# Kernel tuning notes

Hardware: AMD Instinct MI355X
Metric: run time of the kernel (lower is better)

The kernel has to match this reference:

```python
import jax, jax.numpy as jnp
import numpy as np

W_CUB = 0.1
W_CD = 1.0
W_EXT = 0.01
W_SPS = 0.01
THRED = 24.0
COS_EPS = 1e-4

# cube face buffers (6 faces x 3 coords)
MASK_PROJECT = jnp.array([[0,1,1],[0,1,1],[1,0,1],[1,0,1],[1,1,0],[1,1,0]], jnp.float32)
MASK_PLANE   = jnp.array([[1,0,0],[1,0,0],[0,1,0],[0,1,0],[0,0,1],[0,0,1]], jnp.float32)
CUBE_NORMAL  = jnp.array([[-1,0,0],[1,0,0],[0,-1,0],[0,1,0],[0,0,-1],[0,0,1]], jnp.float32)
# torch repeat(...,3,...) of [[-1,-1,-1],[1,1,1]] tiles it -> [c0,c1,c0,c1,c0,c1]
CUBE_PLANES6 = jnp.tile(jnp.array([[-1.,-1.,-1.],[1.,1.,1.]], jnp.float32), (3,1))


def setup_inputs():
    B, P, N, S = 4, 24, 3072, 128
    key = jax.random.key(0)
    ks = jax.random.split(key, 8)
    pc_inver = jax.random.normal(ks[0], (B, P, N, 3), jnp.float32)
    normals_inver = jax.random.normal(ks[1], (B, P, N, 3), jnp.float32)
    scale = jax.random.uniform(ks[2], (B, P, 3), jnp.float32) * 0.9 + 0.1
    shape = jax.random.uniform(ks[3], (B, P, 2), jnp.float32) * 1.3 + 0.2
    exist = jax.random.uniform(ks[4], (B, P, 1), jnp.float32) * 0.98 + 0.01
    assign_matrix = jax.nn.softmax(jax.random.normal(ks[5], (B, N, P), jnp.float32), axis=-1)
    etas = jax.random.uniform(ks[6], (B, P, S), jnp.float32, minval=-jnp.pi/2, maxval=jnp.pi/2)
    omegas = jax.random.uniform(ks[7], (B, P, S), jnp.float32, minval=-jnp.pi, maxval=jnp.pi)
    return dict(pc_inver=pc_inver, normals_inver=normals_inver, scale=scale,
                shape=shape, exist=exist, assign_matrix=assign_matrix,
                etas=etas, omegas=omegas)


def _fexp(x, p):
    return jnp.sign(x) * jnp.abs(x) ** p


def _sample_sq_points(scale, eps, etas, omegas):
    # scale (B,P,3), eps (B,P,2), etas/omegas (B,P,S) -> (B,P,S,3)
    etas = jnp.where(etas == 0, 1e-6, etas)
    omegas = jnp.where(omegas == 0, 1e-6, omegas)
    a1, a2, a3 = scale[..., 0:1], scale[..., 1:2], scale[..., 2:3]
    e1, e2 = eps[..., 0:1], eps[..., 1:2]
    ce, se = jnp.cos(etas), jnp.sin(etas)
    co, so = jnp.cos(omegas), jnp.sin(omegas)
    x = a1 * _fexp(ce, e1) * _fexp(co, e2)
    y = a2 * _fexp(ce, e1) * _fexp(so, e2)
    z = a3 * _fexp(se, e1)
    fix = lambda v: (jnp.where(v > 0, 1.0, -1.0)) * jnp.maximum(jnp.abs(v), 1e-6)
    return jnp.stack([fix(x), fix(y), fix(z)], -1)


def _cd_loss(pc_inver, scale, shape, exist, assign_matrix, etas, omegas):
    X = _sample_sq_points(scale, shape, etas, omegas)          # (B,P,S,3)
    diff = X[:, :, :, None, :] - pc_inver[:, :, None, :, :]    # (B,P,S,N,3)
    D = jnp.sum(diff * diff, -1)                               # (B,P,S,N)
    pcl2prim = jnp.min(D, axis=2)                              # (B,P,N)
    pcl_loss = jnp.mean(jnp.sum(jnp.swapaxes(pcl2prim, 1, 2) * assign_matrix, -1))
    prim2pcl = jnp.mean(jnp.min(D, axis=3), axis=-1)           # (B,P)
    e = exist[..., 0]
    prim_loss = jnp.mean(jnp.sum(prim2pcl * e, -1) / (jnp.sum(e, -1) + 1e-6))
    return pcl_loss, prim_loss


def _cuboid_loss(pc_inver, normals_inver, scale, assign_matrix):
    pc = jnp.swapaxes(pc_inver, 1, 2)        # (B,N,P,3)
    nrm = jnp.swapaxes(normals_inver, 1, 2)  # (B,N,P,3)
    n_norm = jnp.maximum(jnp.linalg.norm(nrm, axis=-1, keepdims=True), COS_EPS)
    cos = jnp.einsum('bnpc,fc->bnpf', nrm, CUBE_NORMAL) / n_norm  # ||cube_normal||=1
    idx = jnp.argmax(cos, axis=-1)           # (B,N,P)
    s = scale[:, None, :, None, :]           # (B,1,P,1,3)
    proj = pc[:, :, :, None, :] * MASK_PROJECT + (CUBE_PLANES6 * s) * MASK_PLANE  # (B,N,P,6,3)
    proj = jnp.clip(proj, -s, s)
    proj_sel = jnp.take_along_axis(proj, idx[..., None, None], axis=3)[..., 0, :]  # (B,N,P,3)
    d = jnp.sum((proj_sel - pc) ** 2, -1)    # (B,N,P)
    return jnp.mean(jnp.sum(d * assign_matrix, -1))


def _common_losses(assign_matrix, exist):
    gt = jax.lax.stop_gradient((jnp.sum(assign_matrix, 1) > THRED).astype(jnp.float32))  # (B,P)
    p = exist[..., 0]
    bce = -jnp.mean(gt * jnp.log(p) + (1.0 - gt) * jnp.log1p(-p))
    N = assign_matrix.shape[1]
    sps = jnp.mean(jnp.mean(jnp.sqrt(jnp.sum(assign_matrix, 1) / N + 0.01), -1) ** 2)
    return bce, sps


def reference(pc_inver, normals_inver, scale, shape, exist, assign_matrix, etas, omegas):
    cub = _cuboid_loss(pc_inver, normals_inver, scale, assign_matrix)
    pcl_loss, prim_loss = _cd_loss(pc_inver, scale, shape, exist, assign_matrix, etas, omegas)
    bce, sps = _common_losses(assign_matrix, exist)
    return W_CUB * cub + W_CD * (pcl_loss + prim_loss) + W_EXT * bce + W_SPS * sps
```

## Files before the change

### kernel.cpp

```cpp
#include <hip/hip_runtime.h>
#include <math.h>

#define BB 4
#define PP 24
#define NN 3072
#define SS 128
#define CHUNK 512
#define NSPLIT 6
#define PART_STRIDE 132

__device__ __forceinline__ float fexp_f(float v, float p) {
    float m = powf(fabsf(v), p);
    float s = (v > 0.f) ? 1.f : ((v < 0.f) ? -1.f : 0.f);
    return s * m;
}
__device__ __forceinline__ float fix_f(float v) {
    return ((v > 0.f) ? 1.f : -1.f) * fmaxf(fabsf(v), 1e-6f);
}
__device__ __forceinline__ float wave_sum(float v) {
    #pragma unroll
    for (int off = 32; off > 0; off >>= 1) v += __shfl_down(v, off);
    return v;
}
__device__ __forceinline__ float cub_dist(float px, float py, float pz,
                                          float nx, float ny, float nz,
                                          float sc0, float sc1, float sc2) {
    float best = -nx; int idx = 0;
    if ( nx > best) { best =  nx; idx = 1; }
    if (-ny > best) { best = -ny; idx = 2; }
    if ( ny > best) { best =  ny; idx = 3; }
    if (-nz > best) { best = -nz; idx = 4; }
    if ( nz > best) { best =  nz; idx = 5; }
    const int c = idx >> 1;
    const float scc = (c == 0) ? sc0 : ((c == 1) ? sc1 : sc2);
    const float fv  = (idx & 1) ? scc : -scc;
    float pr0 = (c == 0) ? fv : fminf(fmaxf(px, -sc0), sc0);
    float pr1 = (c == 1) ? fv : fminf(fmaxf(py, -sc1), sc1);
    float pr2 = (c == 2) ? fv : fminf(fmaxf(pz, -sc2), sc2);
    float d0 = pr0 - px, d1 = pr1 - py, d2 = pr2 - pz;
    return fmaf(d0, d0, fmaf(d1, d1, d2 * d2));
}

__global__ __launch_bounds__(256) void superdec_main(
    const float* __restrict__ pc, const float* __restrict__ nrm,
    const float* __restrict__ scale, const float* __restrict__ shape,
    const float* __restrict__ assign,
    const float* __restrict__ etas, const float* __restrict__ omegas,
    float* __restrict__ ws)
{
    const int blk   = blockIdx.x;
    const int bp    = blk / NSPLIT;
    const int split = blk % NSPLIT;
    const int b     = bp / PP;
    const int p     = bp % PP;
    const int tid   = threadIdx.x;
    const int n0    = split * CHUNK;

    __shared__ float4 Xs[SS];
    __shared__ float4 Pts[CHUNK];
    __shared__ float  red[CHUNK];
    __shared__ float  wsum[12];

    const float sc0 = scale[bp * 3 + 0];
    const float sc1 = scale[bp * 3 + 1];
    const float sc2 = scale[bp * 3 + 2];

    if (tid < SS) {
        const float e1 = shape[bp * 2 + 0];
        const float e2 = shape[bp * 2 + 1];
        float eta = etas[bp * SS + tid];
        float omg = omegas[bp * SS + tid];
        eta = (eta == 0.f) ? 1e-6f : eta;
        omg = (omg == 0.f) ? 1e-6f : omg;
        float ce = cosf(eta), se = sinf(eta);
        float co = cosf(omg), so = sinf(omg);
        float fce = fexp_f(ce, e1);
        float x = fix_f(sc0 * fce * fexp_f(co, e2));
        float y = fix_f(sc1 * fce * fexp_f(so, e2));
        float z = fix_f(sc2 * fexp_f(se, e1));
        float xsq = fmaf(x, x, fmaf(y, y, z * z));
        Xs[tid] = make_float4(-2.f * x, -2.f * y, -2.f * z, xsq);
    }

    const float* pcb = pc  + ((size_t)bp * NN + n0) * 3;
    const float* nrb = nrm + ((size_t)bp * NN + n0) * 3;
    const int iA = tid, iB = tid + 256;
    const float pxA = pcb[iA * 3 + 0], pyA = pcb[iA * 3 + 1], pzA = pcb[iA * 3 + 2];
    const float pxB = pcb[iB * 3 + 0], pyB = pcb[iB * 3 + 1], pzB = pcb[iB * 3 + 2];
    const float psqA = fmaf(pxA, pxA, fmaf(pyA, pyA, pzA * pzA));
    const float psqB = fmaf(pxB, pxB, fmaf(pyB, pyB, pzB * pzB));
    Pts[iA] = make_float4(pxA, pyA, pzA, psqA);
    Pts[iB] = make_float4(pxB, pyB, pzB, psqB);
    const float amA = assign[((size_t)b * NN + n0 + iA) * PP + p];
    const float amB = assign[((size_t)b * NN + n0 + iB) * PP + p];
    const float nxA = nrb[iA * 3 + 0], nyA = nrb[iA * 3 + 1], nzA = nrb[iA * 3 + 2];
    const float nxB = nrb[iB * 3 + 0], nyB = nrb[iB * 3 + 1], nzB = nrb[iB * 3 + 2];
    __syncthreads();

    float mA0 = 3.4e38f, mA1 = 3.4e38f, mB0 = 3.4e38f, mB1 = 3.4e38f;
    #pragma unroll 4
    for (int s = 0; s < SS; s += 2) {
        float4 x0 = Xs[s + 0];
        float4 x1 = Xs[s + 1];
        float d;
        d = fmaf(x0.x, pxA, fmaf(x0.y, pyA, fmaf(x0.z, pzA, x0.w))); mA0 = fminf(mA0, d);
        d = fmaf(x1.x, pxA, fmaf(x1.y, pyA, fmaf(x1.z, pzA, x1.w))); mA1 = fminf(mA1, d);
        d = fmaf(x0.x, pxB, fmaf(x0.y, pyB, fmaf(x0.z, pzB, x0.w))); mB0 = fminf(mB0, d);
        d = fmaf(x1.x, pxB, fmaf(x1.y, pyB, fmaf(x1.z, pzB, x1.w))); mB1 = fminf(mB1, d);
    }
    const float dminA = fminf(mA0, mA1) + psqA;
    const float dminB = fminf(mB0, mB1) + psqB;
    float acc_pcl = dminA * amA + dminB * amB;
    float acc_cub = cub_dist(pxA, pyA, pzA, nxA, nyA, nzA, sc0, sc1, sc2) * amA
                  + cub_dist(pxB, pyB, pzB, nxB, nyB, nzB, sc0, sc1, sc2) * amB;
    float acc_am  = amA + amB;

    {
        float s0 = wave_sum(acc_pcl);
        float s1 = wave_sum(acc_cub);
        float s2 = wave_sum(acc_am);
        const int lane = tid & 63, wave = tid >> 6;
        if (lane == 0) {
            wsum[wave * 3 + 0] = s0;
            wsum[wave * 3 + 1] = s1;
            wsum[wave * 3 + 2] = s2;
        }
    }

    {
        const int sA = tid & 63;
        const int q  = tid >> 6;
        const float4 xa = Xs[sA];
        const float4 xb = Xs[sA + 64];
        const int nb0 = q * (CHUNK / 4);
        float ma0 = 3.4e38f, ma1 = 3.4e38f, mb0 = 3.4e38f, mb1 = 3.4e38f;
        #pragma unroll 4
        for (int n = 0; n < CHUNK / 4; n += 2) {
            float4 p0 = Pts[nb0 + n];
            float4 p1 = Pts[nb0 + n + 1];
            float d;
            d = fmaf(xa.x, p0.x, fmaf(xa.y, p0.y, fmaf(xa.z, p0.z, p0.w))); ma0 = fminf(ma0, d);
            d = fmaf(xa.x, p1.x, fmaf(xa.y, p1.y, fmaf(xa.z, p1.z, p1.w))); ma1 = fminf(ma1, d);
            d = fmaf(xb.x, p0.x, fmaf(xb.y, p0.y, fmaf(xb.z, p0.z, p0.w))); mb0 = fminf(mb0, d);
            d = fmaf(xb.x, p1.x, fmaf(xb.y, p1.y, fmaf(xb.z, p1.z, p1.w))); mb1 = fminf(mb1, d);
        }
        red[q * 128 + sA]      = fminf(ma0, ma1);
        red[q * 128 + 64 + sA] = fminf(mb0, mb1);
    }
    __syncthreads();

    float* part = ws + (size_t)(bp * NSPLIT + split) * PART_STRIDE;
    if (tid < SS) {
        float m = fminf(fminf(red[tid], red[128 + tid]),
                        fminf(red[256 + tid], red[384 + tid]));
        part[tid] = m + Xs[tid].w;
    }
    if (tid == 0) {
        part[SS + 0] = wsum[0] + wsum[3] + wsum[6] + wsum[9];
        part[SS + 1] = wsum[1] + wsum[4] + wsum[7] + wsum[10];
        part[SS + 2] = wsum[2] + wsum[5] + wsum[8] + wsum[11];
    }
}

__global__ __launch_bounds__(1024) void superdec_reduce_final(
    const float* __restrict__ ws, const float* __restrict__ exist,
    float* __restrict__ out)
{
    __shared__ float s_prim[96];
    __shared__ float s_pcl[96], s_cub[96], s_bce[96], s_e[96], s_sq[96];
    const int t    = threadIdx.x;
    const int lane = t & 63;
    if (t < 96) s_prim[t] = 0.f;
    __syncthreads();

    #pragma unroll
    for (int k = 0; k < (96 * 128) / 1024; ++k) {
        const int idx = t + k * 1024;
        const int bp  = idx >> 7;
        const int s   = idx & 127;
        const float* base = ws + (size_t)bp * (NSPLIT * PART_STRIDE) + s;
        float m = fminf(fminf(fminf(base[0 * PART_STRIDE], base[1 * PART_STRIDE]),
                              fminf(base[2 * PART_STRIDE], base[3 * PART_STRIDE])),
                        fminf(base[4 * PART_STRIDE], base[5 * PART_STRIDE]));
        float sm = wave_sum(m);
        if (lane == 0) atomicAdd(&s_prim[bp], sm);
    }

    if (t < 96) {
        const float* base = ws + (size_t)t * (NSPLIT * PART_STRIDE) + SS;
        float pcl = 0.f, cub = 0.f, cs = 0.f;
        #pragma unroll
        for (int sp = 0; sp < NSPLIT; ++sp) {
            pcl += base[sp * PART_STRIDE + 0];
            cub += base[sp * PART_STRIDE + 1];
            cs  += base[sp * PART_STRIDE + 2];
        }
        const float e  = exist[t];
        const float gt = (cs > 24.0f) ? 1.f : 0.f;
        s_pcl[t] = pcl;
        s_cub[t] = cub;
        s_bce[t] = gt * logf(e) + (1.f - gt) * log1pf(-e);
        s_e[t]   = e;
        s_sq[t]  = sqrtf(cs / (float)NN + 0.01f);
    }
    __syncthreads();

    if (t == 0) {
        float pcl_sum = 0.f, cub_sum = 0.f, bce_sum = 0.f, prim_loss = 0.f, sps = 0.f;
        #pragma unroll
        for (int b_ = 0; b_ < BB; ++b_) {
            float pe = 0.f, ee = 0.f, sq = 0.f;
            #pragma unroll
            for (int p_ = 0; p_ < PP; ++p_) {
                const int i = b_ * PP + p_;
                pcl_sum += s_pcl[i];
                cub_sum += s_cub[i];
                bce_sum += s_bce[i];
                pe += (s_prim[i] / (float)SS) * s_e[i];
                ee += s_e[i];
                sq += s_sq[i];
            }
            prim_loss += pe / (ee + 1e-6f);
            float mb = sq / (float)PP;
            sps += mb * mb;
        }
        prim_loss /= (float)BB;
        sps       /= (float)BB;
        float pcl_loss = pcl_sum / (float)(BB * NN);
        float cub      = cub_sum / (float)(BB * NN);
        float bce      = -bce_sum / (float)(BB * PP);
        out[0] = 0.1f * cub + 1.0f * (pcl_loss + prim_loss) + 0.01f * bce + 0.01f * sps;
    }
}

extern "C" void kernel_launch(void* const* d_in, const int* in_sizes, int n_in,
                              void* d_out, int out_size, void* d_ws, size_t ws_size,
                              hipStream_t stream) {
    const float* pc     = (const float*)d_in[0];
    const float* nrm    = (const float*)d_in[1];
    const float* scale  = (const float*)d_in[2];
    const float* shape  = (const float*)d_in[3];
    const float* exist  = (const float*)d_in[4];
    const float* assign = (const float*)d_in[5];
    const float* etas   = (const float*)d_in[6];
    const float* omegas = (const float*)d_in[7];
    float* ws  = (float*)d_ws;
    float* out = (float*)d_out;

    superdec_main<<<BB * PP * NSPLIT, 256, 0, stream>>>(
        pc, nrm, scale, shape, assign, etas, omegas, ws);
    superdec_reduce_final<<<1, 1024, 0, stream>>>(ws, exist, out);
}
```

Measured before the change: 95.54 us.

## Register-tile both min-distance passes and vectorize point/normal loads

Each thread now loads 4 consecutive points and normals as three float4 vector loads instead of scalar strided loads. The point-to-sample pass splits the sample set across two halves of the block, with 4 points per thread, and merges partial minima through shared memory. The sample-to-point pass uses 4 samples by 64 points per thread with an 8-way final reduction. The aim is more reuse per shared-memory read and fewer global transactions. The cost is more registers, an extra barrier, and half the threads sitting idle during setup and the cuboid/assignment work.

Result: no change. 94.43 us (-1.2%).

```diff
diff --git a/kernel.cpp b/kernel.cpp
--- a/kernel.cpp
+++ b/kernel.cpp
@@ -8,6 +8,7 @@
 #define CHUNK 512
 #define NSPLIT 6
 #define PART_STRIDE 132
+#define FINF 3.4e38f
 
 __device__ __forceinline__ float fexp_f(float v, float p) {
     float m = powf(fabsf(v), p);
@@ -55,67 +56,103 @@
     const int p     = bp % PP;
     const int tid   = threadIdx.x;
     const int n0    = split * CHUNK;
+    const int pid   = tid & 127;
+    const int q     = tid >> 7;
 
     __shared__ float4 Xs[SS];
     __shared__ float4 Pts[CHUNK];
-    __shared__ float  red[CHUNK];
-    __shared__ float  wsum[12];
+    __shared__ float4 dmin2[2][128];
+    __shared__ float  red[8 * SS];
+    __shared__ float  wsum[6];
 
     const float sc0 = scale[bp * 3 + 0];
     const float sc1 = scale[bp * 3 + 1];
     const float sc2 = scale[bp * 3 + 2];
 
-    if (tid < SS) {
-        const float e1 = shape[bp * 2 + 0];
-        const float e2 = shape[bp * 2 + 1];
-        float eta = etas[bp * SS + tid];
-        float omg = omegas[bp * SS + tid];
-        eta = (eta == 0.f) ? 1e-6f : eta;
-        omg = (omg == 0.f) ? 1e-6f : omg;
-        float ce = cosf(eta), se = sinf(eta);
-        float co = cosf(omg), so = sinf(omg);
-        float fce = fexp_f(ce, e1);
-        float x = fix_f(sc0 * fce * fexp_f(co, e2));
-        float y = fix_f(sc1 * fce * fexp_f(so, e2));
-        float z = fix_f(sc2 * fexp_f(se, e1));
-        float xsq = fmaf(x, x, fmaf(y, y, z * z));
-        Xs[tid] = make_float4(-2.f * x, -2.f * y, -2.f * z, xsq);
-    }
-
-    const float* pcb = pc  + ((size_t)bp * NN + n0) * 3;
-    const float* nrb = nrm + ((size_t)bp * NN + n0) * 3;
-    const int iA = tid, iB = tid + 256;
-    const float pxA = pcb[iA * 3 + 0], pyA = pcb[iA * 3 + 1], pzA = pcb[iA * 3 + 2];
-    const float pxB = pcb[iB * 3 + 0], pyB = pcb[iB * 3 + 1], pzB = pcb[iB * 3 + 2];
-    const float psqA = fmaf(pxA, pxA, fmaf(pyA, pyA, pzA * pzA));
-    const float psqB = fmaf(pxB, pxB, fmaf(pyB, pyB, pzB * pzB));
-    Pts[iA] = make_float4(pxA, pyA, pzA, psqA);
-    Pts[iB] = make_float4(pxB, pyB, pzB, psqB);
-    const float amA = assign[((size_t)b * NN + n0 + iA) * PP + p];
-    const float amB = assign[((size_t)b * NN + n0 + iB) * PP + p];
-    const float nxA = nrb[iA * 3 + 0], nyA = nrb[iA * 3 + 1], nzA = nrb[iA * 3 + 2];
-    const float nxB = nrb[iB * 3 + 0], nyB = nrb[iB * 3 + 1], nzB = nrb[iB * 3 + 2];
-    __syncthreads();
-
-    float mA0 = 3.4e38f, mA1 = 3.4e38f, mB0 = 3.4e38f, mB1 = 3.4e38f;
-    #pragma unroll 4
-    for (int s = 0; s < SS; s += 2) {
-        float4 x0 = Xs[s + 0];
-        float4 x1 = Xs[s + 1];
-        float d;
-        d = fmaf(x0.x, pxA, fmaf(x0.y, pyA, fmaf(x0.z, pzA, x0.w))); mA0 = fminf(mA0, d);
-        d = fmaf(x1.x, pxA, fmaf(x1.y, pyA, fmaf(x1.z, pzA, x1.w))); mA1 = fminf(mA1, d);
-        d = fmaf(x0.x, pxB, fmaf(x0.y, pyB, fmaf(x0.z, pzB, x0.w))); mB0 = fminf(mB0, d);
-        d = fmaf(x1.x, pxB, fmaf(x1.y, pyB, fmaf(x1.z, pzB, x1.w))); mB1 = fminf(mB1, d);
-    }
-    const float dminA = fminf(mA0, mA1) + psqA;
-    const float dminB = fminf(mB0, mB1) + psqB;
-    float acc_pcl = dminA * amA + dminB * amB;
-    float acc_cub = cub_dist(pxA, pyA, pzA, nxA, nyA, nzA, sc0, sc1, sc2) * amA
-                  + cub_dist(pxB, pyB, pzB, nxB, nyB, nzB, sc0, sc1, sc2) * amB;
-    float acc_am  = amA + amB;
+    const float4* pc4 = (const float4*)(pc + ((size_t)bp * NN + n0) * 3);
+    const float4 g0 = pc4[pid * 3 + 0];
+    const float4 g1 = pc4[pid * 3 + 1];
+    const float4 g2 = pc4[pid * 3 + 2];
+    const float px0 = g0.x, py0 = g0.y, pz0 = g0.z;
+    const float px1 = g0.w, py1 = g1.x, pz1 = g1.y;
+    const float px2 = g1.z, py2 = g1.w, pz2 = g2.x;
+    const float px3 = g2.y, py3 = g2.z, pz3 = g2.w;
+    const float ps0 = fmaf(px0, px0, fmaf(py0, py0, pz0 * pz0));
+    const float ps1 = fmaf(px1, px1, fmaf(py1, py1, pz1 * pz1));
+    const float ps2 = fmaf(px2, px2, fmaf(py2, py2, pz2 * pz2));
+    const float ps3 = fmaf(px3, px3, fmaf(py3, py3, pz3 * pz3));
+
+    float cub0 = 0.f, cub1 = 0.f, cub2 = 0.f, cub3 = 0.f;
+    float am0 = 0.f, am1 = 0.f, am2 = 0.f, am3 = 0.f;
+
+    if (q == 0) {
+        {
+            const float e1 = shape[bp * 2 + 0];
+            const float e2 = shape[bp * 2 + 1];
+            float eta = etas[bp * SS + tid];
+            float omg = omegas[bp * SS + tid];
+            eta = (eta == 0.f) ? 1e-6f : eta;
+            omg = (omg == 0.f) ? 1e-6f : omg;
+            float ce = cosf(eta), se = sinf(eta);
+            float co = cosf(omg), so = sinf(omg);
+            float fce = fexp_f(ce, e1);
+            float x = fix_f(sc0 * fce * fexp_f(co, e2));
+            float y = fix_f(sc1 * fce * fexp_f(so, e2));
+            float z = fix_f(sc2 * fexp_f(se, e1));
+            float xsq = fmaf(x, x, fmaf(y, y, z * z));
+            Xs[tid] = make_float4(-2.f * x, -2.f * y, -2.f * z, xsq);
+        }
+        Pts[pid * 4 + 0] = make_float4(px0, py0, pz0, ps0);
+        Pts[pid * 4 + 1] = make_float4(px1, py1, pz1, ps1);
+        Pts[pid * 4 + 2] = make_float4(px2, py2, pz2, ps2);
+        Pts[pid * 4 + 3] = make_float4(px3, py3, pz3, ps3);
+        const float4* nr4 = (const float4*)(nrm + ((size_t)bp * NN + n0) * 3);
+        const float4 h0 = nr4[pid * 3 + 0];
+        const float4 h1 = nr4[pid * 3 + 1];
+        const float4 h2 = nr4[pid * 3 + 2];
+        cub0 = cub_dist(px0, py0, pz0, h0.x, h0.y, h0.z, sc0, sc1, sc2);
+        cub1 = cub_dist(px1, py1, pz1, h0.w, h1.x, h1.y, sc0, sc1, sc2);
+        cub2 = cub_dist(px2, py2, pz2, h1.z, h1.w, h2.x, sc0, sc1, sc2);
+        cub3 = cub_dist(px3, py3, pz3, h2.y, h2.z, h2.w, sc0, sc1, sc2);
+        const size_t abase = ((size_t)b * NN + n0 + pid * 4) * PP + p;
+        am0 = assign[abase + 0 * PP];
+        am1 = assign[abase + 1 * PP];
+        am2 = assign[abase + 2 * PP];
+        am3 = assign[abase + 3 * PP];
+    }
+    __syncthreads();
 
     {
+        const int sb = q * 64;
+        float m0 = FINF, m1 = FINF, m2 = FINF, m3 = FINF;
+        #pragma unroll 4
+        for (int s = 0; s < 64; s += 2) {
+            float4 xa = Xs[sb + s];
+            float4 xb = Xs[sb + s + 1];
+            float d;
+            d = fmaf(xa.x, px0, fmaf(xa.y, py0, fmaf(xa.z, pz0, xa.w))); m0 = fminf(m0, d);
+            d = fmaf(xa.x, px1, fmaf(xa.y, py1, fmaf(xa.z, pz1, xa.w))); m1 = fminf(m1, d);
+            d = fmaf(xa.x, px2, fmaf(xa.y, py2, fmaf(xa.z, pz2, xa.w))); m2 = fminf(m2, d);
+            d = fmaf(xa.x, px3, fmaf(xa.y, py3, fmaf(xa.z, pz3, xa.w))); m3 = fminf(m3, d);
+            d = fmaf(xb.x, px0, fmaf(xb.y, py0, fmaf(xb.z, pz0, xb.w))); m0 = fminf(m0, d);
+            d = fmaf(xb.x, px1, fmaf(xb.y, py1, fmaf(xb.z, pz1, xb.w))); m1 = fminf(m1, d);
+            d = fmaf(xb.x, px2, fmaf(xb.y, py2, fmaf(xb.z, pz2, xb.w))); m2 = fminf(m2, d);
+            d = fmaf(xb.x, px3, fmaf(xb.y, py3, fmaf(xb.z, pz3, xb.w))); m3 = fminf(m3, d);
+        }
+        dmin2[q][pid] = make_float4(m0, m1, m2, m3);
+    }
+    __syncthreads();
+
+    if (q == 0) {
+        float4 a = dmin2[0][pid];
+        float4 c = dmin2[1][pid];
+        float d0 = fminf(a.x, c.x) + ps0;
+        float d1 = fminf(a.y, c.y) + ps1;
+        float d2 = fminf(a.z, c.z) + ps2;
+        float d3 = fminf(a.w, c.w) + ps3;
+        float acc_pcl = d0 * am0 + d1 * am1 + d2 * am2 + d3 * am3;
+        float acc_cub = cub0 * am0 + cub1 * am1 + cub2 * am2 + cub3 * am3;
+        float acc_am  = am0 + am1 + am2 + am3;
         float s0 = wave_sum(acc_pcl);
         float s1 = wave_sum(acc_cub);
         float s2 = wave_sum(acc_am);
@@ -128,37 +165,46 @@
     }
 
     {
-        const int sA = tid & 63;
-        const int q  = tid >> 6;
-        const float4 xa = Xs[sA];
-        const float4 xb = Xs[sA + 64];
-        const int nb0 = q * (CHUNK / 4);
-        float ma0 = 3.4e38f, ma1 = 3.4e38f, mb0 = 3.4e38f, mb1 = 3.4e38f;
+        const int rep = tid >> 5;
+        const int sb  = tid & 31;
+        const float4 x0 = Xs[sb];
+        const float4 x1 = Xs[sb + 32];
+        const float4 x2 = Xs[sb + 64];
+        const float4 x3 = Xs[sb + 96];
+        const int nb = rep * 64;
+        float r0 = FINF, r1 = FINF, r2 = FINF, r3 = FINF;
         #pragma unroll 4
-        for (int n = 0; n < CHUNK / 4; n += 2) {
-            float4 p0 = Pts[nb0 + n];
-            float4 p1 = Pts[nb0 + n + 1];
+        for (int n = 0; n < 64; n += 2) {
+            float4 pa = Pts[nb + n];
+            float4 pb = Pts[nb + n + 1];
             float d;
-            d = fmaf(xa.x, p0.x, fmaf(xa.y, p0.y, fmaf(xa.z, p0.z, p0.w))); ma0 = fminf(ma0, d);
-            d = fmaf(xa.x, p1.x, fmaf(xa.y, p1.y, fmaf(xa.z, p1.z, p1.w))); ma1 = fminf(ma1, d);
-            d = fmaf(xb.x, p0.x, fmaf(xb.y, p0.y, fmaf(xb.z, p0.z, p0.w))); mb0 = fminf(mb0, d);
-            d = fmaf(xb.x, p1.x, fmaf(xb.y, p1.y, fmaf(xb.z, p1.z, p1.w))); mb1 = fminf(mb1, d);
-        }
-        red[q * 128 + sA]      = fminf(ma0, ma1);
-        red[q * 128 + 64 + sA] = fminf(mb0, mb1);
+            d = fmaf(x0.x, pa.x, fmaf(x0.y, pa.y, fmaf(x0.z, pa.z, pa.w))); r0 = fminf(r0, d);
+            d = fmaf(x1.x, pa.x, fmaf(x1.y, pa.y, fmaf(x1.z, pa.z, pa.w))); r1 = fminf(r1, d);
+            d = fmaf(x2.x, pa.x, fmaf(x2.y, pa.y, fmaf(x2.z, pa.z, pa.w))); r2 = fminf(r2, d);
+            d = fmaf(x3.x, pa.x, fmaf(x3.y, pa.y, fmaf(x3.z, pa.z, pa.w))); r3 = fminf(r3, d);
+            d = fmaf(x0.x, pb.x, fmaf(x0.y, pb.y, fmaf(x0.z, pb.z, pb.w))); r0 = fminf(r0, d);
+            d = fmaf(x1.x, pb.x, fmaf(x1.y, pb.y, fmaf(x1.z, pb.z, pb.w))); r1 = fminf(r1, d);
+            d = fmaf(x2.x, pb.x, fmaf(x2.y, pb.y, fmaf(x2.z, pb.z, pb.w))); r2 = fminf(r2, d);
+            d = fmaf(x3.x, pb.x, fmaf(x3.y, pb.y, fmaf(x3.z, pb.z, pb.w))); r3 = fminf(r3, d);
+        }
+        red[rep * SS + sb +  0] = r0;
+        red[rep * SS + sb + 32] = r1;
+        red[rep * SS + sb + 64] = r2;
+        red[rep * SS + sb + 96] = r3;
     }
     __syncthreads();
 
     float* part = ws + (size_t)(bp * NSPLIT + split) * PART_STRIDE;
     if (tid < SS) {
-        float m = fminf(fminf(red[tid], red[128 + tid]),
-                        fminf(red[256 + tid], red[384 + tid]));
+        float m = red[tid];
+        #pragma unroll
+        for (int r = 1; r < 8; ++r) m = fminf(m, red[r * SS + tid]);
         part[tid] = m + Xs[tid].w;
     }
     if (tid == 0) {
-        part[SS + 0] = wsum[0] + wsum[3] + wsum[6] + wsum[9];
-        part[SS + 1] = wsum[1] + wsum[4] + wsum[7] + wsum[10];
-        part[SS + 2] = wsum[2] + wsum[5] + wsum[8] + wsum[11];
+        part[SS + 0] = wsum[0] + wsum[3];
+        part[SS + 1] = wsum[1] + wsum[4];
+        part[SS + 2] = wsum[2] + wsum[5];
     }
 }
 
```
